# Optimization experiments

Measured on AMD Instinct MI355X. Metric: run time of the kernel, lower is better.

Reference implementation:

```python
import jax, jax.numpy as jnp
import numpy as np

START_IDX = 1  # PAD_IDX = 0, END_IDX = 2 (unused in teacher-forcing path)
B, N, F = 16, 49, 1024
H, E, V = 1024, 1024, 15000
S, W = 5, 12


def setup_inputs() -> dict:
    key = jax.random.key(0)
    ks = jax.random.split(key, 16)
    def w(k, shape, s=0.02):
        return jax.random.normal(k, shape, dtype=jnp.float32) * s
    emb = w(ks[0], (V, E)).at[0].set(0.0)  # padding_idx = 0
    return dict(
        features=jax.random.normal(ks[1], (B, N, F), dtype=jnp.float32),
        reports=jax.random.randint(ks[2], (B, S, W), 0, V),
        attn_w1=w(ks[3], (F + H, H)), attn_b1=jnp.zeros((H,), jnp.float32),
        attn_w2=w(ks[4], (H, 1)), attn_b2=jnp.zeros((1,), jnp.float32),
        s_wih=w(ks[5], (4 * H, F)), s_whh=w(ks[6], (4 * H, H)),
        s_bih=jnp.zeros((4 * H,), jnp.float32), s_bhh=jnp.zeros((4 * H,), jnp.float32),
        stop_w=w(ks[7], (H, 1)), stop_b=jnp.zeros((1,), jnp.float32),
        emb=emb,
        w_wih=w(ks[8], (4 * H, E)), w_whh=w(ks[9], (4 * H, H)),
        w_bih=jnp.zeros((4 * H,), jnp.float32), w_bhh=jnp.zeros((4 * H,), jnp.float32),
        fc_w=w(ks[10], (H, V)), fc_b=jnp.zeros((V,), jnp.float32),
    )


def _lstm_cell(x, h, c, wih, whh, bih, bhh):
    # PyTorch LSTMCell: gates ordered i, f, g, o
    gates = x @ wih.T + h @ whh.T + (bih + bhh)
    i, f, g, o = jnp.split(gates, 4, axis=-1)
    c = jax.nn.sigmoid(f) * c + jax.nn.sigmoid(i) * jnp.tanh(g)
    h = jax.nn.sigmoid(o) * jnp.tanh(c)
    return h, c


def _attention(features, h, w1, b1, w2, b2):
    # features [B,N,F], h [B,H] -> additive 2-layer attention over N locations
    b, n, _ = features.shape
    hcat = jnp.broadcast_to(h[:, None, :], (b, n, h.shape[-1]))
    x = jnp.concatenate([features, hcat], axis=-1)           # [B,N,F+H]
    e = (jnp.tanh(x @ w1 + b1) @ w2 + b2)[..., 0]            # [B,N]
    scores = jax.nn.softmax(e, axis=-1)
    att = jnp.einsum('bn,bnf->bf', scores, features)          # [B,F]
    return att, scores


def _forward(features, reports, attn_w1, attn_b1, attn_w2, attn_b2,
             s_wih, s_whh, s_bih, s_bhh, stop_w, stop_b, emb,
             w_wih, w_whh, w_bih, w_bhh, fc_w, fc_b):
    bsz = features.shape[0]
    h0 = jnp.zeros((bsz, s_whh.shape[-1]), features.dtype)
    att0, _ = _attention(features, h0, attn_w1, attn_b1, attn_w2, attn_b2)
    start_emb = jnp.broadcast_to(emb[START_IDX][None, :], (bsz, emb.shape[-1]))

    def sentence_step(carry, reports_i):   # reports_i: [W, B] teacher-forcing tokens
        h, c, att = carry
        h, c = _lstm_cell(att, h, c, s_wih, s_whh, s_bih, s_bhh)
        czero = jnp.zeros_like(h)

        def word_step(wc, idx):
            hw, cw, inp = wc
            hw, cw = _lstm_cell(inp, hw, cw, w_wih, w_whh, w_bih, w_bhh)
            pred = hw @ fc_w + fc_b                           # [B,V]
            return (hw, cw, emb[idx]), pred

        # word LSTM initialized with h=topic, c=0; first input = <start> embedding
        _, preds = jax.lax.scan(word_step, (h, czero, start_emb), reports_i)  # [W,B,V]
        stop = jax.nn.sigmoid(h @ stop_w + stop_b)[:, 0]      # [B]
        att, scores = _attention(features, h, attn_w1, attn_b1, attn_w2, attn_b2)
        return (h, c, att), (preds, stop, scores)

    reports_sw = jnp.transpose(reports, (1, 2, 0))            # [S,W,B]
    _, (seq, stops, scores) = jax.lax.scan(sentence_step, (h0, h0, att0), reports_sw)
    seq_out = jnp.transpose(seq, (2, 0, 1, 3))                # [B,S,W,V]
    stops_out = jnp.transpose(stops, (1, 0))                  # [B,S]
    scores_out = jnp.transpose(scores, (1, 0, 2))             # [B,S,N]
    return seq_out, stops_out, scores_out


def reference(features, reports, attn_w1, attn_b1, attn_w2, attn_b2,
              s_wih, s_whh, s_bih, s_bhh, stop_w, stop_b, emb,
              w_wih, w_whh, w_bih, w_bhh, fc_w, fc_b):
    return _forward(features, reports, attn_w1, attn_b1, attn_w2, attn_b2,
                    s_wih, s_whh, s_bih, s_bhh, stop_w, stop_b, emb,
                    w_wih, w_whh, w_bih, w_bhh, fc_w, fc_b)
```

## Files before the change

kernel.cpp:

```cpp
#include <hip/hip_runtime.h>
#include <hip/hip_bf16.h>

#define B_  16
#define S_  5
#define W_  12
#define NL_ 49
#define H_  1024
#define V_  15000
#define SEQ_N   14400000
#define STOP_N  80
#define OUT_STOP (SEQ_N)
#define OUT_SCORE (SEQ_N + STOP_N)

typedef __attribute__((ext_vector_type(8))) short     short8;
typedef __attribute__((ext_vector_type(4))) float     f32x4;
typedef __attribute__((ext_vector_type(4))) unsigned int u32x4;
typedef __attribute__((ext_vector_type(4))) unsigned short us4;

#define OFF_FCWT   0ull
#define OFF_WWHHP  30720000ull
#define OFF_WWIHP  39108608ull
#define OFF_WSCATP 47497216ull
#define OFF_W1AT   64274432ull
#define OFF_W1BT   66371584ull
#define OFF_FBF    68468736ull
#define OFF_XIN    70074368ull
#define OFF_PF     72040448ull
#define OFF_XW     75251712ull
#define OFF_HBALL  90980352ull
#define OFF_HWBF0  92946432ull
#define OFF_HWBF1  93110272ull
#define OFF_ACAT1  93274112ull
#define OFF_H      93339648ull
#define OFF_EVAL   93405184ull
#define OFF_ACAT0  93408384ull
#define OFF_C      93473920ull
#define OFF_CW     93539456ull
#define OFF_HPROJ  93867136ull
#define WS_TOTAL   93932672ull
#define ZERO_BASE  OFF_ACAT0
#define ZERO_BYTES (524288ull)

__device__ __forceinline__ unsigned short f2bf(float x){
  unsigned u = __float_as_uint(x);
  u += 0x7fffu + ((u >> 16) & 1u);
  return (unsigned short)(u >> 16);
}
__device__ __forceinline__ float sigm(float x){ return 1.f/(1.f+expf(-x)); }

typedef __attribute__((address_space(3))) unsigned int  as3_u32;
typedef __attribute__((address_space(1))) const unsigned int as1_u32;

__device__ __forceinline__ void gl16(const void* g, void* l){
  __builtin_amdgcn_global_load_lds((as1_u32*)g, (as3_u32*)l, 16, 0, 0);
}

template<int ROWS,int CH,int NW>
__device__ __forceinline__ void stage_swz(const unsigned short* __restrict__ gbase, int grs,
                                          unsigned short* lds, int wid, int lane,
                                          int r0, int rmax){
  constexpr int RPI = 64/CH;
  constexpr int NISS = ROWS/RPI;
  const int r_in = lane / CH;
  const int cbp  = lane % CH;
  #pragma unroll
  for (int it = wid; it < NISS; it += NW){
    int rl = it*RPI + r_in;
    int gr = r0 + rl; gr = gr < rmax ? gr : rmax-1;
    int cb = cbp ^ (rl & 7);
    gl16(gbase + (size_t)gr*grs + cb*8, lds + it*RPI*CH*8);
  }
}

__global__ void k_cvt(const float* __restrict__ src, unsigned short* __restrict__ dst, int n){
  int idx = (blockIdx.x*256 + threadIdx.x)*4;
  if (idx >= n) return;
  f32x4 v = *(const f32x4*)(src + idx);
  us4 o; o[0]=f2bf(v[0]); o[1]=f2bf(v[1]); o[2]=f2bf(v[2]); o[3]=f2bf(v[3]);
  *(us4*)(dst + idx) = o;
}

__global__ void k_cvt_gate(const float* __restrict__ src, unsigned short* __restrict__ dst,
                           int dld, int doff){
  int idx = (blockIdx.x*256 + threadIdx.x)*4;
  int n = idx >> 10, cc = idx & 1023;
  int gate = (n >> 4) & 3, j = ((n >> 6) << 4) | (n & 15);
  f32x4 v = *(const f32x4*)(src + ((size_t)(gate*1024 + j) << 10) + cc);
  us4 o; o[0]=f2bf(v[0]); o[1]=f2bf(v[1]); o[2]=f2bf(v[2]); o[3]=f2bf(v[3]);
  *(us4*)(dst + (size_t)n*dld + doff + cc) = o;
}

__global__ void k_transp(const float* __restrict__ src, int sld, int r0, int R, int Cc,
                         unsigned short* __restrict__ dst, int dld){
  __shared__ float t[32][33];
  int rb = blockIdx.x*32, cb = blockIdx.y*32;
  int tx = threadIdx.x & 31, ty = threadIdx.x >> 5;
  for (int i = ty; i < 32; i += 8){
    int r = rb + i, c = cb + tx;
    t[i][tx] = (r < R && c < Cc) ? src[(size_t)(r0 + r)*sld + c] : 0.f;
  }
  __syncthreads();
  for (int i = ty; i < 32; i += 8){
    int c = cb + i, r = rb + tx;
    if (c < Cc && r < R) dst[(size_t)c*dld + r] = f2bf(t[tx][i]);
  }
}

__global__ void k_gather(const float* __restrict__ emb, const int* __restrict__ reports,
                         unsigned short* __restrict__ Xin){
  int m = blockIdx.x;
  int w = m / 80, r = m % 80, s = r >> 4, b = r & 15;
  int tok = (w == 0) ? 1 : reports[b*60 + s*12 + (w-1)];
  const float* src = emb + ((size_t)tok << 10);
  int k = threadIdx.x * 4;
  f32x4 v = *(const f32x4*)(src + k);
  us4 o; o[0]=f2bf(v[0]); o[1]=f2bf(v[1]); o[2]=f2bf(v[2]); o[3]=f2bf(v[3]);
  *(us4*)(Xin + (size_t)m*1024 + k) = o;
}

template<int BM,int BN,int BK,int WM,int WN,int EPI>
__global__ void k_gemm(const unsigned short* __restrict__ A, int lda,
                       const unsigned short* __restrict__ Bt, int ldb,
                       float* __restrict__ C, int ldc,
                       const float* __restrict__ bias,
                       int M, int N, int K)
{
  constexpr int NWV = WM*WN;
  constexpr int CH = BK/8;
  __shared__ __align__(16) unsigned short As[BM*BK];
  __shared__ __align__(16) unsigned short Bs[BN*BK];
  const int n0 = blockIdx.x * BN, m0 = blockIdx.y * BM;
  if (n0 >= N) return;
  const int tid  = threadIdx.x;
  const int lane = tid & 63;
  const int wave = tid >> 6;
  constexpr int WROWS = BM/WM, WCOLS = BN/WN;
  constexpr int FM = WROWS/16, FN = WCOLS/16;
  const int wm = wave / WN, wn = wave % WN;
  const int g = lane >> 4, fr = lane & 15;
  const int sx = fr & 7;

  f32x4 acc[FM][FN];
  #pragma unroll
  for (int a=0;a<FM;a++)
    #pragma unroll
    for (int b=0;b<FN;b++) acc[a][b] = (f32x4){0.f,0.f,0.f,0.f};

  for (int k0 = 0; k0 < K; k0 += BK) {
    if (k0) __syncthreads();
    stage_swz<BM,CH,NWV>(A + k0, lda, As, wave, lane, m0, M);
    stage_swz<BN,CH,NWV>(Bt + k0, ldb, Bs, wave, lane, n0, N);
    __syncthreads();
    #pragma unroll
    for (int kk = 0; kk < BK; kk += 32) {
      const int so = ((kk/8 + g) ^ sx) * 8;
      short8 af[FM], bt[FN];
      #pragma unroll
      for (int fm=0; fm<FM; fm++)
        af[fm] = *(const short8*)(As + (wm*WROWS + fm*16 + fr)*BK + so);
      #pragma unroll
      for (int fn=0; fn<FN; fn++)
        bt[fn] = *(const short8*)(Bs + (wn*WCOLS + fn*16 + fr)*BK + so);
      #pragma unroll
      for (int fm=0; fm<FM; fm++)
        #pragma unroll
        for (int fn=0; fn<FN; fn++)
          acc[fm][fn] = __builtin_amdgcn_mfma_f32_16x16x32_bf16(af[fm], bt[fn], acc[fm][fn], 0, 0, 0);
    }
  }

  #pragma unroll
  for (int fm=0; fm<FM; fm++)
    #pragma unroll
    for (int fn=0; fn<FN; fn++)
      #pragma unroll
      for (int j=0; j<4; j++){
        int m = m0 + wm*WROWS + fm*16 + g*4 + j;
        int n = n0 + wn*WCOLS + fn*16 + fr;
        if (m < M && n < N) {
          float v = acc[fm][fn][j];
          if (EPI == 1 || EPI == 2) v += bias[n];
          if (EPI == 2) {
            int b = m & 15, s = (m >> 4) % 5, w = m / 80;
            __builtin_nontemporal_store(v, &C[(size_t)((b*5 + s)*12 + w)*V_ + n]);
          } else if (EPI == 3) {
            __builtin_nontemporal_store(v, &C[(size_t)m*ldc + n]);
          } else {
            C[(size_t)m*ldc + n] = v;
          }
        }
      }
}

template<int BM,int BN,int BK,int WN,int SENT>
__global__ void k_gemm_cell(const unsigned short* __restrict__ A, int lda,
                            const unsigned short* __restrict__ Bt, int ldb,
                            const float* __restrict__ Xg, int ldx,
                            const float* __restrict__ bih, const float* __restrict__ bhh,
                            float* __restrict__ cst,
                            unsigned short* __restrict__ h1, int ldh1,
                            unsigned short* __restrict__ h2,
                            float* __restrict__ hf,
                            int M, int K)
{
  constexpr int CH = BK/8;
  __shared__ __align__(16) unsigned short As[BM*BK];
  __shared__ __align__(16) unsigned short Bs[BN*BK];
  const int tid  = threadIdx.x;
  const int lane = tid & 63;
  const int wn   = tid >> 6;
  const int n0 = blockIdx.x * BN, m0 = blockIdx.y * BM;
  const int g = lane >> 4, fr = lane & 15;
  const int sx = fr & 7;

  f32x4 acc[4];
  #pragma unroll
  for (int b=0;b<4;b++) acc[b] = (f32x4){0.f,0.f,0.f,0.f};

  for (int k0 = 0; k0 < K; k0 += BK) {
    if (k0) __syncthreads();
    stage_swz<BM,CH,WN>(A + k0, lda, As, wn, lane, m0, M);
    stage_swz<BN,CH,WN>(Bt + k0, ldb, Bs, wn, lane, n0, 4096);
    __syncthreads();
    #pragma unroll
    for (int kk = 0; kk < BK; kk += 32) {
      const int so = ((kk/8 + g) ^ sx) * 8;
      short8 af = *(const short8*)(As + fr*BK + so);
      #pragma unroll
      for (int fn=0; fn<4; fn++){
        short8 bt = *(const short8*)(Bs + (wn*64 + fn*16 + fr)*BK + so);
        acc[fn] = __builtin_amdgcn_mfma_f32_16x16x32_bf16(af, bt, acc[fn], 0, 0, 0);
      }
    }
  }

  const int nb = n0 + wn*64 + fr;
  const int j  = ((n0 + wn*64) >> 2) + fr;
  const float b0 = bih[j]        + bhh[j];
  const float b1 = bih[1024 + j] + bhh[1024 + j];
  const float b2 = bih[2048 + j] + bhh[2048 + j];
  const float b3 = bih[3072 + j] + bhh[3072 + j];
  #pragma unroll
  for (int jj=0; jj<4; jj++){
    int m = m0 + g*4 + jj;
    if (m < M){
      float gi = acc[0][jj] + b0;
      float gf = acc[1][jj] + b1;
      float gg = acc[2][jj] + b2;
      float go = acc[3][jj] + b3;
      if (!SENT){
        const float* xg = Xg + (size_t)m*ldx + nb;
        gi += xg[0]; gf += xg[16]; gg += xg[32]; go += xg[48];
      }
      float cn = sigm(gf)*cst[m*1024 + j] + sigm(gi)*tanhf(gg);
      float hn = sigm(go)*tanhf(cn);
      cst[m*1024 + j] = cn;
      unsigned short hb = f2bf(hn);
      h1[(size_t)m*ldh1 + j] = hb;
      h2[(size_t)m*1024 + j] = hb;
      if (SENT) hf[m*1024 + j] = hn;
    }
  }
}

__global__ void k_attn_e(const float* __restrict__ PF, const float* __restrict__ hproj,
                         const float* __restrict__ w2, float* __restrict__ evals)
{
  const int bn = blockIdx.x;
  const int b  = bn / NL_;
  const int tid = threadIdx.x;
  __shared__ float red[4];
  const float* pf = PF + ((size_t)bn << 10);
  const float* hp = hproj + (b << 10);
  int k = tid * 4;
  f32x4 a = *(const f32x4*)(pf + k);
  f32x4 hh = *(const f32x4*)(hp + k);
  f32x4 w = *(const f32x4*)(w2 + k);
  float p = tanhf(a[0]+hh[0])*w[0] + tanhf(a[1]+hh[1])*w[1]
          + tanhf(a[2]+hh[2])*w[2] + tanhf(a[3]+hh[3])*w[3];
  #pragma unroll
  for (int o = 32; o; o >>= 1) p += __shfl_down(p, o, 64);
  if ((tid & 63) == 0) red[tid >> 6] = p;
  __syncthreads();
  if (tid == 0) evals[bn] = red[0] + red[1] + red[2] + red[3];
}

template<int INIT>
__global__ void k_attn_fin(const float* __restrict__ evals, const float* __restrict__ features,
                           const float* __restrict__ h, const float* __restrict__ stop_w,
                           const float* __restrict__ stop_b,
                           unsigned short* __restrict__ Acat, float* __restrict__ outp, int s)
{
  const int b = blockIdx.x, tid = threadIdx.x;
  __shared__ float scs[64];
  __shared__ float red[4];
  if (tid < 64){
    float e = (tid < NL_) ? evals[b*NL_ + tid] : -1e30f;
    float mx = e;
    #pragma unroll
    for (int o = 32; o; o >>= 1) mx = fmaxf(mx, __shfl_xor(mx, o, 64));
    float ex = (tid < NL_) ? expf(e - mx) : 0.f;
    float dn = ex;
    #pragma unroll
    for (int o = 32; o; o >>= 1) dn += __shfl_xor(dn, o, 64);
    float sc = ex / dn;
    if (tid < NL_){
      scs[tid] = sc;
      if (!INIT) outp[OUT_SCORE + (b*5 + s)*NL_ + tid] = sc;
    }
  }
  __syncthreads();
  {
    int f0 = tid * 4;
    f32x4 a = (f32x4){0.f,0.f,0.f,0.f};
    const float* fb = features + (((size_t)b*NL_) << 10) + f0;
    #pragma unroll 7
    for (int n = 0; n < NL_; n++){
      f32x4 v = *(const f32x4*)(fb + ((size_t)n << 10));
      float sc = scs[n];
      a[0] += sc*v[0]; a[1] += sc*v[1]; a[2] += sc*v[2]; a[3] += sc*v[3];
    }
    us4 o4; o4[0]=f2bf(a[0]); o4[1]=f2bf(a[1]); o4[2]=f2bf(a[2]); o4[3]=f2bf(a[3]);
    *(us4*)(Acat + b*2048 + f0) = o4;
  }
  if (!INIT){
    int k = tid * 4;
    f32x4 hv = *(const f32x4*)(h + (b << 10) + k);
    f32x4 sw = *(const f32x4*)(stop_w + k);
    float p = hv[0]*sw[0] + hv[1]*sw[1] + hv[2]*sw[2] + hv[3]*sw[3];
    #pragma unroll
    for (int o = 32; o; o >>= 1) p += __shfl_down(p, o, 64);
    if ((tid & 63) == 0) red[tid >> 6] = p;
    __syncthreads();
    if (tid == 0) outp[OUT_STOP + b*5 + s] = sigm(red[0]+red[1]+red[2]+red[3] + stop_b[0]);
  }
}

extern "C" void kernel_launch(void* const* d_in, const int* in_sizes, int n_in,
                              void* d_out, int out_size, void* d_ws, size_t ws_size,
                              hipStream_t stream)
{
  const float* features = (const float*)d_in[0];
  const int*   reports  = (const int*)d_in[1];
  const float* attn_w1  = (const float*)d_in[2];
  const float* attn_b1  = (const float*)d_in[3];
  const float* attn_w2  = (const float*)d_in[4];
  const float* s_wih    = (const float*)d_in[6];
  const float* s_whh    = (const float*)d_in[7];
  const float* s_bih    = (const float*)d_in[8];
  const float* s_bhh    = (const float*)d_in[9];
  const float* stop_w   = (const float*)d_in[10];
  const float* stop_b   = (const float*)d_in[11];
  const float* emb      = (const float*)d_in[12];
  const float* w_wih    = (const float*)d_in[13];
  const float* w_whh    = (const float*)d_in[14];
  const float* w_bih    = (const float*)d_in[15];
  const float* w_bhh    = (const float*)d_in[16];
  const float* fc_w     = (const float*)d_in[17];
  const float* fc_b     = (const float*)d_in[18];
  float* out = (float*)d_out;
  char*  ws  = (char*)d_ws;
  if (ws_size < WS_TOTAL) return;

  unsigned short* FCWT   = (unsigned short*)(ws + OFF_FCWT);
  unsigned short* WWHHP  = (unsigned short*)(ws + OFF_WWHHP);
  unsigned short* WWIHP  = (unsigned short*)(ws + OFF_WWIHP);
  unsigned short* WSCATP = (unsigned short*)(ws + OFF_WSCATP);
  unsigned short* W1AT   = (unsigned short*)(ws + OFF_W1AT);
  unsigned short* W1BT   = (unsigned short*)(ws + OFF_W1BT);
  unsigned short* FBF    = (unsigned short*)(ws + OFF_FBF);
  unsigned short* XIN    = (unsigned short*)(ws + OFF_XIN);
  float*          PF     = (float*)(ws + OFF_PF);
  float*          XW     = (float*)(ws + OFF_XW);
  unsigned short* HBALL  = (unsigned short*)(ws + OFF_HBALL);
  unsigned short* HW0    = (unsigned short*)(ws + OFF_HWBF0);
  unsigned short* HW1    = (unsigned short*)(ws + OFF_HWBF1);
  unsigned short* ACAT0  = (unsigned short*)(ws + OFF_ACAT0);
  unsigned short* ACAT1  = (unsigned short*)(ws + OFF_ACAT1);
  float*          Hst    = (float*)(ws + OFF_H);
  float*          Cst    = (float*)(ws + OFF_C);
  float*          CW     = (float*)(ws + OFF_CW);
  float*          HPROJ  = (float*)(ws + OFF_HPROJ);
  float*          EVAL   = (float*)(ws + OFF_EVAL);

  hipMemsetAsync(ws + ZERO_BASE, 0, ZERO_BYTES, stream);

  k_cvt<<<784, 256, 0, stream>>>(features, FBF, 802816);
  k_cvt_gate<<<4096, 256, 0, stream>>>(w_whh, WWHHP, 1024, 0);
  k_cvt_gate<<<4096, 256, 0, stream>>>(w_wih, WWIHP, 1024, 0);
  k_cvt_gate<<<4096, 256, 0, stream>>>(s_wih, WSCATP, 2048, 0);
  k_cvt_gate<<<4096, 256, 0, stream>>>(s_whh, WSCATP, 2048, 1024);
  k_transp<<<dim3(32,32),  256, 0, stream>>>(attn_w1, 1024, 0,    1024, 1024,  W1AT, 1024);
  k_transp<<<dim3(32,32),  256, 0, stream>>>(attn_w1, 1024, 1024, 1024, 1024,  W1BT, 1024);
  k_transp<<<dim3(32,469), 256, 0, stream>>>(fc_w,   15000, 0,    1024, 15000, FCWT, 1024);
  k_gather<<<960, 256, 0, stream>>>(emb, reports, XIN);

  k_gemm<64,64,128,2,2,1><<<dim3(16,13), 256, 0, stream>>>(FBF,1024, W1AT,1024, PF,1024, attn_b1, 784,1024,1024);
  k_gemm<64,128,128,2,2,3><<<dim3(32,15), 256, 0, stream>>>(XIN,1024, WWIHP,1024, XW,4096, nullptr, 960,4096,1024);

  k_attn_e<<<784, 256, 0, stream>>>(PF, HPROJ, attn_w2, EVAL);
  k_attn_fin<1><<<16, 256, 0, stream>>>(EVAL, features, Hst, stop_w, stop_b, ACAT0, out, 0);

  unsigned short* ACS[2] = {ACAT0, ACAT1};
  for (int s = 0; s < S_; s++){
    unsigned short* cur = ACS[s & 1];
    unsigned short* nxt = ACS[(s + 1) & 1];
    k_gemm_cell<16,128,128,2,1><<<dim3(32,1), 128, 0, stream>>>(
        cur, 2048, WSCATP, 2048, nullptr, 0, s_bih, s_bhh, Cst,
        nxt + 1024, 2048, HW0 + s*16*1024, Hst, 16, 2048);
    k_gemm<16,64,256,1,4,0><<<dim3(16,1), 256, 0, stream>>>(
        nxt + 1024, 2048, W1BT, 1024, HPROJ, 1024, nullptr, 16, 1024, 1024);
    k_attn_e<<<784, 256, 0, stream>>>(PF, HPROJ, attn_w2, EVAL);
    k_attn_fin<0><<<16, 256, 0, stream>>>(EVAL, features, Hst, stop_w, stop_b, nxt, out, s);
  }

  unsigned short* HW[2] = {HW0, HW1};
  for (int w = 0; w < W_; w++){
    k_gemm_cell<16,128,128,2,0><<<dim3(32,5), 128, 0, stream>>>(
        HW[w & 1], 1024, WWHHP, 1024, XW + (size_t)w*80*4096, 4096, w_bih, w_bhh, CW,
        HW[(w + 1) & 1], 1024, HBALL + (size_t)w*80*1024, nullptr, 80, 1024);
  }

  k_gemm<128,128,64,2,2,2><<<dim3(120,8), 256, 0, stream>>>(HBALL,1024, FCWT,1024, out,V_, fc_b, 960,15000,1024);
}
```

Baseline: 559.1 us.

## Merge all prep kernels into one launch and fuse attention energy with softmax

```diff
diff --git a/kernel.cpp b/kernel.cpp
--- a/kernel.cpp
+++ b/kernel.cpp
@@ -72,17 +72,10 @@
   }
 }
 
-__global__ void k_cvt(const float* __restrict__ src, unsigned short* __restrict__ dst, int n){
-  int idx = (blockIdx.x*256 + threadIdx.x)*4;
-  if (idx >= n) return;
-  f32x4 v = *(const f32x4*)(src + idx);
-  us4 o; o[0]=f2bf(v[0]); o[1]=f2bf(v[1]); o[2]=f2bf(v[2]); o[3]=f2bf(v[3]);
-  *(us4*)(dst + idx) = o;
-}
-
-__global__ void k_cvt_gate(const float* __restrict__ src, unsigned short* __restrict__ dst,
-                           int dld, int doff){
-  int idx = (blockIdx.x*256 + threadIdx.x)*4;
+__device__ __forceinline__ void cvt_gate_blk(const float* __restrict__ src,
+                                             unsigned short* __restrict__ dst,
+                                             int blk, int dld, int doff){
+  int idx = (blk*256 + threadIdx.x)*4;
   int n = idx >> 10, cc = idx & 1023;
   int gate = (n >> 4) & 3, j = ((n >> 6) << 4) | (n & 15);
   f32x4 v = *(const f32x4*)(src + ((size_t)(gate*1024 + j) << 10) + cc);
@@ -90,32 +83,79 @@
   *(us4*)(dst + (size_t)n*dld + doff + cc) = o;
 }
 
-__global__ void k_transp(const float* __restrict__ src, int sld, int r0, int R, int Cc,
-                         unsigned short* __restrict__ dst, int dld){
+#define P0 784
+#define P1 (P0+4096)
+#define P2 (P1+4096)
+#define P3 (P2+4096)
+#define P4 (P3+4096)
+#define P5 (P4+960)
+#define P6 (P5+2048)
+#define P7 (P6+15008)
+#define P8 (P7+128)
+
+__global__ void k_prep(const float* __restrict__ features,
+                       const float* __restrict__ w_whh, const float* __restrict__ w_wih,
+                       const float* __restrict__ s_wih, const float* __restrict__ s_whh,
+                       const float* __restrict__ emb, const int* __restrict__ reports,
+                       const float* __restrict__ attn_w1, const float* __restrict__ fc_w,
+                       unsigned short* __restrict__ FBF, unsigned short* __restrict__ WWHHP,
+                       unsigned short* __restrict__ WWIHP, unsigned short* __restrict__ WSCATP,
+                       unsigned short* __restrict__ XIN,
+                       unsigned short* __restrict__ W1AT, unsigned short* __restrict__ W1BT,
+                       unsigned short* __restrict__ FCWT, char* __restrict__ zbase)
+{
   __shared__ float t[32][33];
-  int rb = blockIdx.x*32, cb = blockIdx.y*32;
-  int tx = threadIdx.x & 31, ty = threadIdx.x >> 5;
-  for (int i = ty; i < 32; i += 8){
-    int r = rb + i, c = cb + tx;
-    t[i][tx] = (r < R && c < Cc) ? src[(size_t)(r0 + r)*sld + c] : 0.f;
-  }
-  __syncthreads();
-  for (int i = ty; i < 32; i += 8){
-    int c = cb + i, r = rb + tx;
-    if (c < Cc && r < R) dst[(size_t)c*dld + r] = f2bf(t[tx][i]);
-  }
-}
-
-__global__ void k_gather(const float* __restrict__ emb, const int* __restrict__ reports,
-                         unsigned short* __restrict__ Xin){
-  int m = blockIdx.x;
-  int w = m / 80, r = m % 80, s = r >> 4, b = r & 15;
-  int tok = (w == 0) ? 1 : reports[b*60 + s*12 + (w-1)];
-  const float* src = emb + ((size_t)tok << 10);
-  int k = threadIdx.x * 4;
-  f32x4 v = *(const f32x4*)(src + k);
-  us4 o; o[0]=f2bf(v[0]); o[1]=f2bf(v[1]); o[2]=f2bf(v[2]); o[3]=f2bf(v[3]);
-  *(us4*)(Xin + (size_t)m*1024 + k) = o;
+  int bx = blockIdx.x;
+  if (bx < P0){
+    int idx = (bx*256 + threadIdx.x)*4;
+    f32x4 v = *(const f32x4*)(features + idx);
+    us4 o; o[0]=f2bf(v[0]); o[1]=f2bf(v[1]); o[2]=f2bf(v[2]); o[3]=f2bf(v[3]);
+    *(us4*)(FBF + idx) = o;
+  } else if (bx < P1){
+    cvt_gate_blk(w_whh, WWHHP, bx - P0, 1024, 0);
+  } else if (bx < P2){
+    cvt_gate_blk(w_wih, WWIHP, bx - P1, 1024, 0);
+  } else if (bx < P3){
+    cvt_gate_blk(s_wih, WSCATP, bx - P2, 2048, 0);
+  } else if (bx < P4){
+    cvt_gate_blk(s_whh, WSCATP, bx - P3, 2048, 1024);
+  } else if (bx < P5){
+    int m = bx - P4;
+    int w = m / 80, r = m % 80, s = r >> 4, b = r & 15;
+    int tok = (w == 0) ? 1 : reports[b*60 + s*12 + (w-1)];
+    const float* src = emb + ((size_t)tok << 10);
+    int k = threadIdx.x * 4;
+    f32x4 v = *(const f32x4*)(src + k);
+    us4 o; o[0]=f2bf(v[0]); o[1]=f2bf(v[1]); o[2]=f2bf(v[2]); o[3]=f2bf(v[3]);
+    *(us4*)(XIN + (size_t)m*1024 + k) = o;
+  } else if (bx < P6){
+    int idx = bx - P5;
+    int z = idx >> 10, rem = idx & 1023;
+    int rb = (rem & 31)*32, cb = (rem >> 5)*32, r0 = z*1024;
+    unsigned short* dst = z ? W1BT : W1AT;
+    int tx = threadIdx.x & 31, ty = threadIdx.x >> 5;
+    for (int i = ty; i < 32; i += 8)
+      t[i][tx] = attn_w1[(size_t)(r0 + rb + i)*1024 + cb + tx];
+    __syncthreads();
+    for (int i = ty; i < 32; i += 8)
+      dst[(size_t)(cb + i)*1024 + rb + tx] = f2bf(t[tx][i]);
+  } else if (bx < P7){
+    int idx = bx - P6;
+    int rb = (idx & 31)*32, cb = (idx >> 5)*32;
+    int tx = threadIdx.x & 31, ty = threadIdx.x >> 5;
+    for (int i = ty; i < 32; i += 8){
+      int c = cb + tx;
+      t[i][tx] = (c < V_) ? fc_w[(size_t)(rb + i)*V_ + c] : 0.f;
+    }
+    __syncthreads();
+    for (int i = ty; i < 32; i += 8){
+      int c = cb + i;
+      if (c < V_) FCWT[(size_t)c*1024 + rb + tx] = f2bf(t[tx][i]);
+    }
+  } else {
+    int idx = bx - P7;
+    *(u32x4*)(zbase + ((size_t)idx*256 + threadIdx.x)*16) = (u32x4){0u,0u,0u,0u};
+  }
 }
 
 template<int BM,int BN,int BK,int WM,int WN,int EPI>
@@ -263,39 +303,41 @@
   }
 }
 
-__global__ void k_attn_e(const float* __restrict__ PF, const float* __restrict__ hproj,
-                         const float* __restrict__ w2, float* __restrict__ evals)
+template<int INIT>
+__global__ void __launch_bounds__(1024) k_attn2(
+    const float* __restrict__ HPROJ, const float* __restrict__ PF,
+    const float* __restrict__ w2, const float* __restrict__ features,
+    const float* __restrict__ hF, const float* __restrict__ stop_w,
+    const float* __restrict__ stop_b,
+    unsigned short* __restrict__ att_out, float* __restrict__ outp, int s)
 {
-  const int bn = blockIdx.x;
-  const int b  = bn / NL_;
-  const int tid = threadIdx.x;
-  __shared__ float red[4];
-  const float* pf = PF + ((size_t)bn << 10);
-  const float* hp = hproj + (b << 10);
-  int k = tid * 4;
-  f32x4 a = *(const f32x4*)(pf + k);
-  f32x4 hh = *(const f32x4*)(hp + k);
-  f32x4 w = *(const f32x4*)(w2 + k);
-  float p = tanhf(a[0]+hh[0])*w[0] + tanhf(a[1]+hh[1])*w[1]
-          + tanhf(a[2]+hh[2])*w[2] + tanhf(a[3]+hh[3])*w[3];
-  #pragma unroll
-  for (int o = 32; o; o >>= 1) p += __shfl_down(p, o, 64);
-  if ((tid & 63) == 0) red[tid >> 6] = p;
+  __shared__ float hp[1024];
+  __shared__ float ev[64];
+  __shared__ float scs[NL_];
+  __shared__ float red[16];
+  const int b = blockIdx.x, tid = threadIdx.x;
+  const int grp = tid >> 6, lane = tid & 63;
+
+  hp[tid] = INIT ? 0.f : HPROJ[b*1024 + tid];
   __syncthreads();
-  if (tid == 0) evals[bn] = red[0] + red[1] + red[2] + red[3];
-}
-
-template<int INIT>
-__global__ void k_attn_fin(const float* __restrict__ evals, const float* __restrict__ features,
-                           const float* __restrict__ h, const float* __restrict__ stop_w,
-                           const float* __restrict__ stop_b,
-                           unsigned short* __restrict__ Acat, float* __restrict__ outp, int s)
-{
-  const int b = blockIdx.x, tid = threadIdx.x;
-  __shared__ float scs[64];
-  __shared__ float red[4];
+
+  for (int n = grp; n < NL_; n += 16){
+    const float* pf = PF + ((size_t)(b*NL_ + n) << 10);
+    float p = 0.f;
+    for (int k = lane*4; k < 1024; k += 256){
+      f32x4 a = *(const f32x4*)(pf + k);
+      f32x4 w = *(const f32x4*)(w2 + k);
+      p += tanhf(a[0]+hp[k  ])*w[0] + tanhf(a[1]+hp[k+1])*w[1]
+         + tanhf(a[2]+hp[k+2])*w[2] + tanhf(a[3]+hp[k+3])*w[3];
+    }
+    #pragma unroll
+    for (int o = 32; o; o >>= 1) p += __shfl_down(p, o, 64);
+    if (lane == 0) ev[n] = p;
+  }
+  __syncthreads();
+
   if (tid < 64){
-    float e = (tid < NL_) ? evals[b*NL_ + tid] : -1e30f;
+    float e = (tid < NL_) ? ev[tid] : -1e30f;
     float mx = e;
     #pragma unroll
     for (int o = 32; o; o >>= 1) mx = fmaxf(mx, __shfl_xor(mx, o, 64));
@@ -310,29 +352,26 @@
     }
   }
   __syncthreads();
+
   {
-    int f0 = tid * 4;
-    f32x4 a = (f32x4){0.f,0.f,0.f,0.f};
-    const float* fb = features + (((size_t)b*NL_) << 10) + f0;
+    float a = 0.f;
+    const float* fb = features + (((size_t)(b*NL_)) << 10) + tid;
     #pragma unroll 7
-    for (int n = 0; n < NL_; n++){
-      f32x4 v = *(const f32x4*)(fb + ((size_t)n << 10));
-      float sc = scs[n];
-      a[0] += sc*v[0]; a[1] += sc*v[1]; a[2] += sc*v[2]; a[3] += sc*v[3];
-    }
-    us4 o4; o4[0]=f2bf(a[0]); o4[1]=f2bf(a[1]); o4[2]=f2bf(a[2]); o4[3]=f2bf(a[3]);
-    *(us4*)(Acat + b*2048 + f0) = o4;
+    for (int n = 0; n < NL_; n++) a += scs[n] * fb[(size_t)n << 10];
+    att_out[b*2048 + tid] = f2bf(a);
   }
   if (!INIT){
-    int k = tid * 4;
-    f32x4 hv = *(const f32x4*)(h + (b << 10) + k);
-    f32x4 sw = *(const f32x4*)(stop_w + k);
-    float p = hv[0]*sw[0] + hv[1]*sw[1] + hv[2]*sw[2] + hv[3]*sw[3];
+    float p = hF[b*1024 + tid] * stop_w[tid];
     #pragma unroll
     for (int o = 32; o; o >>= 1) p += __shfl_down(p, o, 64);
-    if ((tid & 63) == 0) red[tid >> 6] = p;
+    if (lane == 0) red[grp] = p;
     __syncthreads();
-    if (tid == 0) outp[OUT_STOP + b*5 + s] = sigm(red[0]+red[1]+red[2]+red[3] + stop_b[0]);
+    if (tid == 0){
+      float t = 0.f;
+      #pragma unroll
+      for (int i = 0; i < 16; i++) t += red[i];
+      outp[OUT_STOP + b*5 + s] = sigm(t + stop_b[0]);
+    }
   }
 }
 
@@ -381,25 +420,16 @@
   float*          Cst    = (float*)(ws + OFF_C);
   float*          CW     = (float*)(ws + OFF_CW);
   float*          HPROJ  = (float*)(ws + OFF_HPROJ);
-  float*          EVAL   = (float*)(ws + OFF_EVAL);
-
-  hipMemsetAsync(ws + ZERO_BASE, 0, ZERO_BYTES, stream);
-
-  k_cvt<<<784, 256, 0, stream>>>(features, FBF, 802816);
-  k_cvt_gate<<<4096, 256, 0, stream>>>(w_whh, WWHHP, 1024, 0);
-  k_cvt_gate<<<4096, 256, 0, stream>>>(w_wih, WWIHP, 1024, 0);
-  k_cvt_gate<<<4096, 256, 0, stream>>>(s_wih, WSCATP, 2048, 0);
-  k_cvt_gate<<<4096, 256, 0, stream>>>(s_whh, WSCATP, 2048, 1024);
-  k_transp<<<dim3(32,32),  256, 0, stream>>>(attn_w1, 1024, 0,    1024, 1024,  W1AT, 1024);
-  k_transp<<<dim3(32,32),  256, 0, stream>>>(attn_w1, 1024, 1024, 1024, 1024,  W1BT, 1024);
-  k_transp<<<dim3(32,469), 256, 0, stream>>>(fc_w,   15000, 0,    1024, 15000, FCWT, 1024);
-  k_gather<<<960, 256, 0, stream>>>(emb, reports, XIN);
+
+  k_prep<<<P8, 256, 0, stream>>>(features, w_whh, w_wih, s_wih, s_whh, emb, reports,
+                                 attn_w1, fc_w,
+                                 FBF, WWHHP, WWIHP, WSCATP, XIN, W1AT, W1BT, FCWT,
+                                 ws + ZERO_BASE);
 
   k_gemm<64,64,128,2,2,1><<<dim3(16,13), 256, 0, stream>>>(FBF,1024, W1AT,1024, PF,1024, attn_b1, 784,1024,1024);
   k_gemm<64,128,128,2,2,3><<<dim3(32,15), 256, 0, stream>>>(XIN,1024, WWIHP,1024, XW,4096, nullptr, 960,4096,1024);
 
-  k_attn_e<<<784, 256, 0, stream>>>(PF, HPROJ, attn_w2, EVAL);
-  k_attn_fin<1><<<16, 256, 0, stream>>>(EVAL, features, Hst, stop_w, stop_b, ACAT0, out, 0);
+  k_attn2<1><<<16, 1024, 0, stream>>>(HPROJ, PF, attn_w2, features, Hst, stop_w, stop_b, ACAT0, out, 0);
 
   unsigned short* ACS[2] = {ACAT0, ACAT1};
   for (int s = 0; s < S_; s++){
@@ -410,8 +440,7 @@
         nxt + 1024, 2048, HW0 + s*16*1024, Hst, 16, 2048);
     k_gemm<16,64,256,1,4,0><<<dim3(16,1), 256, 0, stream>>>(
         nxt + 1024, 2048, W1BT, 1024, HPROJ, 1024, nullptr, 16, 1024, 1024);
-    k_attn_e<<<784, 256, 0, stream>>>(PF, HPROJ, attn_w2, EVAL);
-    k_attn_fin<0><<<16, 256, 0, stream>>>(EVAL, features, Hst, stop_w, stop_b, nxt, out, s);
+    k_attn2<0><<<16, 1024, 0, stream>>>(HPROJ, PF, attn_w2, features, Hst, stop_w, stop_b, nxt, out, s);
   }
 
   unsigned short* HW[2] = {HW0, HW1};
```

Result: slower. 593.7 us (+6.2%).
